# Kernel optimization log

Measured on AMD Instinct MI355X. Metric: run time of the kernel, lower is better.

## Reference

```python
import jax, jax.numpy as jnp
import numpy as np
import math

L = 16
F = 2
LOG2_T = 19
T = 1 << LOG2_T            # 524288 entries per level
MIN_RES = 16
MAX_RES = 4096
HASH_INIT_SCALE = 0.001
N_POINTS = 1048576

_growth = math.exp((math.log(MAX_RES) - math.log(MIN_RES)) / (L - 1))
# floor(min_res * growth**l), matching torch buffer level_resolutions
_RES = np.floor(MIN_RES * _growth ** np.arange(L, dtype=np.float64)).astype(np.float32)
_LEVEL_OFFSETS = (np.arange(L, dtype=np.int32) * T)  # (L,)
# hash primes; arithmetic done in uint32 -- low 19 bits match the int64 torch math
_P1 = np.uint32(1)
_P2 = np.uint32(2654435761)
_P3 = np.uint32(805459861)
_MASK = np.uint32(T - 1)


def _hash(ix, iy, iz):
    # ix/iy/iz: int32 grid coords (nonnegative). Returns int32 in [0, T).
    ix = ix.astype(jnp.uint32)
    iy = iy.astype(jnp.uint32)
    iz = iz.astype(jnp.uint32)
    h = (ix * _P1) ^ (iy * _P2) ^ (iz * _P3)
    return (h & _MASK).astype(jnp.int32)


def setup_inputs() -> dict:
    key = jax.random.key(0)
    kx, kt = jax.random.split(key)
    x = jax.random.uniform(kx, (N_POINTS, 3), dtype=jnp.float32)  # in [0,1]
    table = (jax.random.uniform(kt, (T * L, F), dtype=jnp.float32) * 2.0 - 1.0) * HASH_INIT_SCALE
    return {"x": x, "hash_table": table}


def reference(x, hash_table):
    # x: (N, 3) in [0,1]; hash_table: (L*T, F)
    res = jnp.asarray(_RES)                      # (L,)
    offs = jnp.asarray(_LEVEL_OFFSETS)           # (L,)
    scaled = x[:, None, :] * res[None, :, None]  # (N, L, 3)
    floor_f = jnp.floor(scaled)
    frac = scaled - floor_f                      # (N, L, 3)
    fi = floor_f.astype(jnp.int32)               # (N, L, 3)
    wx = frac[..., 0:1]
    wy = frac[..., 1:2]
    wz = frac[..., 2:3]                          # (N, L, 1)
    feats = jnp.zeros(x.shape[:1] + (L, F), dtype=x.dtype)
    for dx in (0, 1):
        for dy in (0, 1):
            for dz in (0, 1):
                idx = _hash(fi[..., 0] + dx, fi[..., 1] + dy, fi[..., 2] + dz)  # (N, L)
                f = hash_table[idx + offs[None, :]]                             # (N, L, F)
                w = ((wx if dx else 1.0 - wx)
                     * (wy if dy else 1.0 - wy)
                     * (wz if dz else 1.0 - wz))                                # (N, L, 1)
                feats = feats + f * w
    return feats.reshape(x.shape[0], L * F)
```

## Files before the change

### kernel.cpp

```cpp
#include <hip/hip_runtime.h>
#include <math.h>

#define NLEVELS 16
#define LOG2_T 19
#define TSIZE (1u << LOG2_T)
#define TMASK (TSIZE - 1u)
#define NPTS 1048576
#define HALFPTS (NPTS / 2)

typedef float vfloat2 __attribute__((ext_vector_type(2)));
typedef float vfloat4 __attribute__((ext_vector_type(4)));

struct Res16 { float r[NLEVELS]; };

__global__ __launch_bounds__(256) void HashGridEncoder_68925635166659_kernel(
    const float* __restrict__ x,
    const vfloat2* __restrict__ table,
    vfloat2* __restrict__ dst,
    const uint32_t mn, const uint32_t ml,
    Res16 res)
{
    const int l = blockIdx.y;
    const int t = blockIdx.x * blockDim.x + threadIdx.x;
    const int nA = t;
    const int nB = t + HALFPTS;

    const float r = res.r[l];
    const vfloat2* __restrict__ tl  = table + (uint32_t)l * TSIZE;
    const vfloat4* __restrict__ tl4 = (const vfloat4*)tl;

    const float pxA = x[3 * nA + 0];
    const float pyA = x[3 * nA + 1];
    const float pzA = x[3 * nA + 2];
    const float pxB = x[3 * nB + 0];
    const float pyB = x[3 * nB + 1];
    const float pzB = x[3 * nB + 2];

    const float sxA = pxA * r, syA = pyA * r, szA = pzA * r;
    const float fxA = floorf(sxA), fyA = floorf(syA), fzA = floorf(szA);
    const float wxA = sxA - fxA, wyA = syA - fyA, wzA = szA - fzA;
    const uint32_t ixA = (uint32_t)(int)fxA;
    const uint32_t iyA = (uint32_t)(int)fyA;
    const uint32_t izA = (uint32_t)(int)fzA;
    const uint32_t hxA1 = ixA + 1u;
    const uint32_t hyA0 = iyA * 2654435761u;
    const uint32_t hyA1 = hyA0 + 2654435761u;
    const uint32_t hzA0 = izA * 805459861u;
    const uint32_t hzA1 = hzA0 + 805459861u;
    const uint32_t bA00 = (ixA ^ hyA0 ^ hzA0) & TMASK;
    const uint32_t bA01 = (ixA ^ hyA0 ^ hzA1) & TMASK;
    const uint32_t bA10 = (ixA ^ hyA1 ^ hzA0) & TMASK;
    const uint32_t bA11 = (ixA ^ hyA1 ^ hzA1) & TMASK;
    const uint32_t eA00 = (hxA1 ^ hyA0 ^ hzA0) & TMASK;
    const uint32_t eA01 = (hxA1 ^ hyA0 ^ hzA1) & TMASK;
    const uint32_t eA10 = (hxA1 ^ hyA1 ^ hzA0) & TMASK;
    const uint32_t eA11 = (hxA1 ^ hyA1 ^ hzA1) & TMASK;

    const float sxB = pxB * r, syB = pyB * r, szB = pzB * r;
    const float fxB = floorf(sxB), fyB = floorf(syB), fzB = floorf(szB);
    const float wxB = sxB - fxB, wyB = syB - fyB, wzB = szB - fzB;
    const uint32_t ixB = (uint32_t)(int)fxB;
    const uint32_t iyB = (uint32_t)(int)fyB;
    const uint32_t izB = (uint32_t)(int)fzB;
    const uint32_t hxB1 = ixB + 1u;
    const uint32_t hyB0 = iyB * 2654435761u;
    const uint32_t hyB1 = hyB0 + 2654435761u;
    const uint32_t hzB0 = izB * 805459861u;
    const uint32_t hzB1 = hzB0 + 805459861u;
    const uint32_t bB00 = (ixB ^ hyB0 ^ hzB0) & TMASK;
    const uint32_t bB01 = (ixB ^ hyB0 ^ hzB1) & TMASK;
    const uint32_t bB10 = (ixB ^ hyB1 ^ hzB0) & TMASK;
    const uint32_t bB11 = (ixB ^ hyB1 ^ hzB1) & TMASK;
    const uint32_t eB00 = (hxB1 ^ hyB0 ^ hzB0) & TMASK;
    const uint32_t eB01 = (hxB1 ^ hyB0 ^ hzB1) & TMASK;
    const uint32_t eB10 = (hxB1 ^ hyB1 ^ hzB0) & TMASK;
    const uint32_t eB11 = (hxB1 ^ hyB1 ^ hzB1) & TMASK;

    const vfloat4 qA00 = tl4[bA00 >> 1];
    const vfloat4 qA01 = tl4[bA01 >> 1];
    const vfloat4 qA10 = tl4[bA10 >> 1];
    const vfloat4 qA11 = tl4[bA11 >> 1];
    const vfloat2 cA100 = tl[eA00];
    const vfloat2 cA101 = tl[eA01];
    const vfloat2 cA110 = tl[eA10];
    const vfloat2 cA111 = tl[eA11];
    const vfloat4 qB00 = tl4[bB00 >> 1];
    const vfloat4 qB01 = tl4[bB01 >> 1];
    const vfloat4 qB10 = tl4[bB10 >> 1];
    const vfloat4 qB11 = tl4[bB11 >> 1];
    const vfloat2 cB100 = tl[eB00];
    const vfloat2 cB101 = tl[eB01];
    const vfloat2 cB110 = tl[eB10];
    const vfloat2 cB111 = tl[eB11];

    const vfloat2 cA000 = (bA00 & 1u) ? vfloat2{qA00.z, qA00.w} : vfloat2{qA00.x, qA00.y};
    const vfloat2 cA001 = (bA01 & 1u) ? vfloat2{qA01.z, qA01.w} : vfloat2{qA01.x, qA01.y};
    const vfloat2 cA010 = (bA10 & 1u) ? vfloat2{qA10.z, qA10.w} : vfloat2{qA10.x, qA10.y};
    const vfloat2 cA011 = (bA11 & 1u) ? vfloat2{qA11.z, qA11.w} : vfloat2{qA11.x, qA11.y};
    const vfloat2 cB000 = (bB00 & 1u) ? vfloat2{qB00.z, qB00.w} : vfloat2{qB00.x, qB00.y};
    const vfloat2 cB001 = (bB01 & 1u) ? vfloat2{qB01.z, qB01.w} : vfloat2{qB01.x, qB01.y};
    const vfloat2 cB010 = (bB10 & 1u) ? vfloat2{qB10.z, qB10.w} : vfloat2{qB10.x, qB10.y};
    const vfloat2 cB011 = (bB11 & 1u) ? vfloat2{qB11.z, qB11.w} : vfloat2{qB11.x, qB11.y};

    {
        const float wx0 = 1.0f - wxA, wy0 = 1.0f - wyA, wz0 = 1.0f - wzA;
        float f0 = 0.0f, f1 = 0.0f, w;
        w = (wx0 * wy0) * wz0; f0 += cA000.x * w; f1 += cA000.y * w;
        w = (wx0 * wy0) * wzA; f0 += cA001.x * w; f1 += cA001.y * w;
        w = (wx0 * wyA) * wz0; f0 += cA010.x * w; f1 += cA010.y * w;
        w = (wx0 * wyA) * wzA; f0 += cA011.x * w; f1 += cA011.y * w;
        w = (wxA * wy0) * wz0; f0 += cA100.x * w; f1 += cA100.y * w;
        w = (wxA * wy0) * wzA; f0 += cA101.x * w; f1 += cA101.y * w;
        w = (wxA * wyA) * wz0; f0 += cA110.x * w; f1 += cA110.y * w;
        w = (wxA * wyA) * wzA; f0 += cA111.x * w; f1 += cA111.y * w;
        vfloat2 v; v.x = f0; v.y = f1;
        __builtin_nontemporal_store(v, dst + (uint32_t)nA * mn + (uint32_t)l * ml);
    }
    {
        const float wx0 = 1.0f - wxB, wy0 = 1.0f - wyB, wz0 = 1.0f - wzB;
        float f0 = 0.0f, f1 = 0.0f, w;
        w = (wx0 * wy0) * wz0; f0 += cB000.x * w; f1 += cB000.y * w;
        w = (wx0 * wy0) * wzB; f0 += cB001.x * w; f1 += cB001.y * w;
        w = (wx0 * wyB) * wz0; f0 += cB010.x * w; f1 += cB010.y * w;
        w = (wx0 * wyB) * wzB; f0 += cB011.x * w; f1 += cB011.y * w;
        w = (wxB * wy0) * wz0; f0 += cB100.x * w; f1 += cB100.y * w;
        w = (wxB * wy0) * wzB; f0 += cB101.x * w; f1 += cB101.y * w;
        w = (wxB * wyB) * wz0; f0 += cB110.x * w; f1 += cB110.y * w;
        w = (wxB * wyB) * wzB; f0 += cB111.x * w; f1 += cB111.y * w;
        vfloat2 v; v.x = f0; v.y = f1;
        __builtin_nontemporal_store(v, dst + (uint32_t)nB * mn + (uint32_t)l * ml);
    }
}

__global__ __launch_bounds__(256) void HashGridEncoder_68925635166659_transpose(
    const vfloat2* __restrict__ ws,
    vfloat4* __restrict__ out4)
{
    __shared__ vfloat2 tile[NLEVELS][33];
    const int t  = threadIdx.x;
    const int p0 = blockIdx.x * 32;

    const int j  = t & 31;
    const int l0 = (t >> 5) * 2;
    tile[l0][j]     = ws[(uint32_t)l0       * NPTS + p0 + j];
    tile[l0 + 1][j] = ws[(uint32_t)(l0 + 1) * NPTS + p0 + j];
    __syncthreads();

    const int p = t >> 3;
    const int c = t & 7;
    const vfloat2 a = tile[2 * c][p];
    const vfloat2 b = tile[2 * c + 1][p];
    vfloat4 v; v.x = a.x; v.y = a.y; v.z = b.x; v.w = b.y;
    __builtin_nontemporal_store(v, out4 + (uint32_t)(p0 + p) * 8 + c);
}

extern "C" void kernel_launch(void* const* d_in, const int* in_sizes, int n_in,
                              void* d_out, int out_size, void* d_ws, size_t ws_size,
                              hipStream_t stream) {
    const float*   x     = (const float*)d_in[0];
    const vfloat2* table = (const vfloat2*)d_in[1];
    vfloat2*       out   = (vfloat2*)d_out;

    Res16 res;
    const double growth = exp((log(4096.0) - log(16.0)) / 15.0);
    for (int l = 0; l < NLEVELS; ++l)
        res.r[l] = (float)floor(16.0 * pow(growth, (double)l));

    const dim3 block(256, 1, 1);
    const dim3 grid(HALFPTS / 256, NLEVELS, 1);

    const size_t ws_needed = (size_t)NLEVELS * NPTS * sizeof(vfloat2);
    if (ws_size >= ws_needed && d_ws != nullptr) {
        vfloat2* ws = (vfloat2*)d_ws;
        HashGridEncoder_68925635166659_kernel<<<grid, block, 0, stream>>>(
            x, table, ws, 1u, (uint32_t)NPTS, res);
        HashGridEncoder_68925635166659_transpose<<<dim3(NPTS / 32, 1, 1), block, 0, stream>>>(
            ws, (vfloat4*)out);
    } else {
        HashGridEncoder_68925635166659_kernel<<<grid, block, 0, stream>>>(
            x, table, out, (uint32_t)NLEVELS, 1u, res);
    }
}
```

Measured before the change: 762.1 us.

## Reuse paired 16B gather for x+1 corners and widen transpose tiles

When the cell's x coordinate is even, the x+1 corner hashes to the neighbouring slot of the same aligned pair already loaded as a 16-byte vector, so the separate 8-byte gathers are skipped and the other half of the pair is selected instead. The transpose kernel now processes 256 points per block with 16-byte nontemporal loads into a larger LDS tile. This cuts random table traffic and transpose launch overhead, at the cost of lane divergence around the conditional loads and more LDS per block.

```diff
diff --git a/kernel.cpp b/kernel.cpp
--- a/kernel.cpp
+++ b/kernel.cpp
@@ -76,22 +76,31 @@
     const uint32_t eB10 = (hxB1 ^ hyB1 ^ hzB0) & TMASK;
     const uint32_t eB11 = (hxB1 ^ hyB1 ^ hzB1) & TMASK;
 
+    vfloat2 cA100, cA101, cA110, cA111;
+    vfloat2 cB100, cB101, cB110, cB111;
+    const uint32_t oddA = ixA & 1u;
+    const uint32_t oddB = ixB & 1u;
+    if (oddA) {
+        cA100 = tl[eA00];
+        cA101 = tl[eA01];
+        cA110 = tl[eA10];
+        cA111 = tl[eA11];
+    }
+    if (oddB) {
+        cB100 = tl[eB00];
+        cB101 = tl[eB01];
+        cB110 = tl[eB10];
+        cB111 = tl[eB11];
+    }
+
     const vfloat4 qA00 = tl4[bA00 >> 1];
     const vfloat4 qA01 = tl4[bA01 >> 1];
     const vfloat4 qA10 = tl4[bA10 >> 1];
     const vfloat4 qA11 = tl4[bA11 >> 1];
-    const vfloat2 cA100 = tl[eA00];
-    const vfloat2 cA101 = tl[eA01];
-    const vfloat2 cA110 = tl[eA10];
-    const vfloat2 cA111 = tl[eA11];
     const vfloat4 qB00 = tl4[bB00 >> 1];
     const vfloat4 qB01 = tl4[bB01 >> 1];
     const vfloat4 qB10 = tl4[bB10 >> 1];
     const vfloat4 qB11 = tl4[bB11 >> 1];
-    const vfloat2 cB100 = tl[eB00];
-    const vfloat2 cB101 = tl[eB01];
-    const vfloat2 cB110 = tl[eB10];
-    const vfloat2 cB111 = tl[eB11];
 
     const vfloat2 cA000 = (bA00 & 1u) ? vfloat2{qA00.z, qA00.w} : vfloat2{qA00.x, qA00.y};
     const vfloat2 cA001 = (bA01 & 1u) ? vfloat2{qA01.z, qA01.w} : vfloat2{qA01.x, qA01.y};
@@ -101,6 +110,19 @@
     const vfloat2 cB001 = (bB01 & 1u) ? vfloat2{qB01.z, qB01.w} : vfloat2{qB01.x, qB01.y};
     const vfloat2 cB010 = (bB10 & 1u) ? vfloat2{qB10.z, qB10.w} : vfloat2{qB10.x, qB10.y};
     const vfloat2 cB011 = (bB11 & 1u) ? vfloat2{qB11.z, qB11.w} : vfloat2{qB11.x, qB11.y};
+
+    if (!oddA) {
+        cA100 = (bA00 & 1u) ? vfloat2{qA00.x, qA00.y} : vfloat2{qA00.z, qA00.w};
+        cA101 = (bA01 & 1u) ? vfloat2{qA01.x, qA01.y} : vfloat2{qA01.z, qA01.w};
+        cA110 = (bA10 & 1u) ? vfloat2{qA10.x, qA10.y} : vfloat2{qA10.z, qA10.w};
+        cA111 = (bA11 & 1u) ? vfloat2{qA11.x, qA11.y} : vfloat2{qA11.z, qA11.w};
+    }
+    if (!oddB) {
+        cB100 = (bB00 & 1u) ? vfloat2{qB00.x, qB00.y} : vfloat2{qB00.z, qB00.w};
+        cB101 = (bB01 & 1u) ? vfloat2{qB01.x, qB01.y} : vfloat2{qB01.z, qB01.w};
+        cB110 = (bB10 & 1u) ? vfloat2{qB10.x, qB10.y} : vfloat2{qB10.z, qB10.w};
+        cB111 = (bB11 & 1u) ? vfloat2{qB11.x, qB11.y} : vfloat2{qB11.z, qB11.w};
+    }
 
     {
         const float wx0 = 1.0f - wxA, wy0 = 1.0f - wyA, wz0 = 1.0f - wzA;
@@ -136,22 +158,31 @@
     const vfloat2* __restrict__ ws,
     vfloat4* __restrict__ out4)
 {
-    __shared__ vfloat2 tile[NLEVELS][33];
+    __shared__ vfloat2 tile[NLEVELS][258];
     const int t  = threadIdx.x;
-    const int p0 = blockIdx.x * 32;
-
-    const int j  = t & 31;
-    const int l0 = (t >> 5) * 2;
-    tile[l0][j]     = ws[(uint32_t)l0       * NPTS + p0 + j];
-    tile[l0 + 1][j] = ws[(uint32_t)(l0 + 1) * NPTS + p0 + j];
+    const int p0 = blockIdx.x * 256;
+
+    const vfloat4* __restrict__ ws4 = (const vfloat4*)ws;
+    #pragma unroll
+    for (int k = 0; k < 8; ++k) {
+        const int lin = k * 256 + t;
+        const int row = lin >> 7;
+        const int col = lin & 127;
+        const vfloat4 v = __builtin_nontemporal_load(
+            ws4 + (size_t)row * (NPTS / 2) + (p0 >> 1) + col);
+        *(vfloat4*)&tile[row][2 * col] = v;
+    }
     __syncthreads();
-
-    const int p = t >> 3;
-    const int c = t & 7;
-    const vfloat2 a = tile[2 * c][p];
-    const vfloat2 b = tile[2 * c + 1][p];
-    vfloat4 v; v.x = a.x; v.y = a.y; v.z = b.x; v.w = b.y;
-    __builtin_nontemporal_store(v, out4 + (uint32_t)(p0 + p) * 8 + c);
+    #pragma unroll
+    for (int k = 0; k < 8; ++k) {
+        const int lin = k * 256 + t;
+        const int p = lin >> 3;
+        const int c = lin & 7;
+        const vfloat2 a = tile[2 * c][p];
+        const vfloat2 b = tile[2 * c + 1][p];
+        vfloat4 v; v.x = a.x; v.y = a.y; v.z = b.x; v.w = b.y;
+        __builtin_nontemporal_store(v, out4 + (size_t)(p0 + p) * 8 + c);
+    }
 }
 
 extern "C" void kernel_launch(void* const* d_in, const int* in_sizes, int n_in,
@@ -174,7 +205,7 @@
         vfloat2* ws = (vfloat2*)d_ws;
         HashGridEncoder_68925635166659_kernel<<<grid, block, 0, stream>>>(
             x, table, ws, 1u, (uint32_t)NPTS, res);
-        HashGridEncoder_68925635166659_transpose<<<dim3(NPTS / 32, 1, 1), block, 0, stream>>>(
+        HashGridEncoder_68925635166659_transpose<<<dim3(NPTS / 256, 1, 1), block, 0, stream>>>(
             ws, (vfloat4*)out);
     } else {
         HashGridEncoder_68925635166659_kernel<<<grid, block, 0, stream>>>(
```

New measurement: 628.6 us. -17.5%, faster.
